# Optimization experiments

Measured on AMD Instinct MI355X. Metric: run time of the kernel, lower is better.

The kernel has to match this reference:

```python
import jax, jax.numpy as jnp
import numpy as np

EPS = 1e-12  # torch F.normalize eps

def _l2norm(x, axis):
    n = jnp.sqrt(jnp.sum(x * x, axis=axis, keepdims=True))
    return x / jnp.maximum(n, EPS)

def setup_inputs() -> dict:
    key = jax.random.key(0)
    k1, k2, k3, k4 = jax.random.split(key, 4)
    B, Lq, Ld, D, NWAY = 128, 32, 180, 128, 8
    query_reps = jax.random.normal(k1, (B, Lq, D), dtype=jnp.float32)
    doc_reps = jax.random.normal(k2, (B, NWAY, Ld, D), dtype=jnp.float32)
    doc_mask = jax.random.randint(k3, (B, NWAY, Ld), 0, 2, dtype=jnp.int32)
    # labels are teacher log-probabilities (KLDivLoss log_target=True)
    labels = jax.nn.log_softmax(jax.random.normal(k4, (B, NWAY), dtype=jnp.float32), axis=-1)
    return {"query_reps": query_reps, "doc_reps": doc_reps, "doc_mask": doc_mask, "labels": labels}

def reference(query_reps, doc_reps, doc_mask, labels):
    # query: L2-normalize over feature dim (dim=2 in torch call)
    q = _l2norm(query_reps, axis=-1)                      # [B, Lq, D]
    # docs: mask padding tokens, then F.normalize with DEFAULT dim=1,
    # i.e. L2-normalize along the token axis (faithful to source).
    d = doc_reps * doc_mask[..., None].astype(doc_reps.dtype)  # [B, W, Ld, D]
    d = _l2norm(d, axis=2)
    # MaxSim: sim[b,w,q,l] = <q_bq, d_bwl>; max over doc tokens, sum over query tokens
    sim = jnp.einsum('bqd,bwld->bwql', q, d)              # [B, W, Lq, Ld]
    scores = jnp.max(sim, axis=-1).sum(axis=-1)           # [B, W]
    log_p = jax.nn.log_softmax(scores, axis=-1)           # == log(softmax(scores))
    # KLDivLoss(log_target=True, reduction='batchmean'): sum(exp(t)*(t - x)) / B
    B = scores.shape[0]
    loss = jnp.sum(jnp.exp(labels) * (labels - log_p)) / B
    return loss  # torch.mean of a scalar is the scalar
```

## Files before the change

### kernel.cpp

```cpp
#include <hip/hip_runtime.h>
#include <math.h>

#define NB 128
#define LQ 32
#define LD 180
#define DD 128
#define NW 8
#define NBW (NB*NW)
#define TP 36

__global__ __launch_bounds__(256) void dnorm_kernel(
    const float* __restrict__ dreps, const int* __restrict__ dmask,
    float* __restrict__ dinv)
{
    __shared__ float s_ssq[8 * DD];
    const int t = threadIdx.x, bw = blockIdx.x;
    const float4* doc4 = (const float4*)(dreps + (size_t)bw * LD * DD);
    const int* mrow = dmask + bw * LD;
    const int d4 = t & 31, rg = t >> 5;
    float sx = 0.f, sy = 0.f, sz = 0.f, sw = 0.f;
    for (int l = rg; l < LD; l += 8) {
        float4 v = doc4[l * 32 + d4];
        float m = (float)mrow[l];
        sx += m * v.x * v.x; sy += m * v.y * v.y;
        sz += m * v.z * v.z; sw += m * v.w * v.w;
    }
    float4 ss; ss.x = sx; ss.y = sy; ss.z = sz; ss.w = sw;
    *(float4*)&s_ssq[rg * DD + 4 * d4] = ss;
    __syncthreads();
    if (t < DD) {
        float tot = 0.f;
        #pragma unroll
        for (int g = 0; g < 8; ++g) tot += s_ssq[g * DD + t];
        dinv[bw * DD + t] = 1.0f / fmaxf(sqrtf(tot), 1e-12f);
    }
}

__global__ __launch_bounds__(256) void qnorm_kernel(
    const float* __restrict__ qreps, float* __restrict__ qinv)
{
    const int t = threadIdx.x, b = blockIdx.x;
    const int r = t >> 3, sub = t & 7;
    const float4* qr = (const float4*)(qreps + (size_t)b * LQ * DD + r * DD + sub * 16);
    float ss = 0.f;
    #pragma unroll
    for (int k = 0; k < 4; ++k) {
        float4 v = qr[k];
        ss += v.x * v.x + v.y * v.y + v.z * v.z + v.w * v.w;
    }
    ss += __shfl_xor(ss, 4);
    ss += __shfl_xor(ss, 2);
    ss += __shfl_xor(ss, 1);
    if (sub == 0) qinv[b * LQ + r] = 1.0f / fmaxf(sqrtf(ss), 1e-12f);
}

__global__ __launch_bounds__(128, 2) void maxsim_kernel(
    const float* __restrict__ qreps, const float* __restrict__ dreps,
    const int* __restrict__ dmask, const float* __restrict__ dinv,
    const float* __restrict__ qinv, float* __restrict__ scores)
{
    __shared__ float s_tile[LD * TP];
    __shared__ float s_q[LQ * TP];
    __shared__ float s_pm[2][LQ];

    const int t = threadIdx.x, bw = blockIdx.x, b = bw >> 3;
    const int lane = t & 63, wave = t >> 6;
    const int rowg = lane >> 4;
    const int colg = lane & 15;
    const int colbase = wave * 84;

    const float4* doc4  = (const float4*)(dreps + (size_t)bw * LD * DD);
    const float4* q4g   = (const float4*)(qreps + (size_t)b * LQ * DD);
    const float4* dinv4 = (const float4*)(dinv + (size_t)bw * DD);
    const float*  qinvb = qinv + b * LQ;

    float acc[8][6];
    #pragma unroll
    for (int k = 0; k < 8; ++k)
        #pragma unroll
        for (int c = 0; c < 6; ++c) acc[k][c] = 0.f;

    for (int cc = 0; cc < 4; ++cc) {
        if (cc) __syncthreads();
        {
            int f = t;
            #pragma unroll
            for (int s = 0; s < 2; ++s, f += 128) {
                int r = f >> 3, d4 = f & 7;
                float4 v  = q4g[r * 32 + cc * 8 + d4];
                float4 di = dinv4[cc * 8 + d4];
                float  qi = qinvb[r];
                v.x *= qi * di.x; v.y *= qi * di.y;
                v.z *= qi * di.z; v.w *= qi * di.w;
                *(float4*)&s_q[r * TP + 4 * d4] = v;
            }
        }
        {
            int f = t;
            #pragma unroll
            for (int s = 0; s < 12; ++s, f += 128) {
                if (f < LD * 8) {
                    int l = f >> 3, d4 = f & 7;
                    *(float4*)&s_tile[l * TP + 4 * d4] = doc4[l * 32 + cc * 8 + d4];
                }
            }
        }
        __syncthreads();

        #pragma unroll
        for (int dq = 0; dq < 8; ++dq) {
            float4 qv[8], tv[6];
            #pragma unroll
            for (int k = 0; k < 8; ++k)
                qv[k] = *(const float4*)&s_q[(rowg + 4 * k) * TP + 4 * dq];
            #pragma unroll
            for (int c = 0; c < 6; ++c)
                tv[c] = *(const float4*)&s_tile[(colbase + colg + 16 * c) * TP + 4 * dq];
            #pragma unroll
            for (int k = 0; k < 8; ++k)
                #pragma unroll
                for (int c = 0; c < 6; ++c) {
                    acc[k][c] = fmaf(qv[k].x, tv[c].x, acc[k][c]);
                    acc[k][c] = fmaf(qv[k].y, tv[c].y, acc[k][c]);
                    acc[k][c] = fmaf(qv[k].z, tv[c].z, acc[k][c]);
                    acc[k][c] = fmaf(qv[k].w, tv[c].w, acc[k][c]);
                }
        }
    }

    int msk[6];
    #pragma unroll
    for (int c = 0; c < 6; ++c)
        msk[c] = dmask[bw * LD + colbase + colg + 16 * c];

    float pm[8];
    #pragma unroll
    for (int k = 0; k < 8; ++k) {
        float m = -INFINITY;
        #pragma unroll
        for (int c = 0; c < 6; ++c) {
            float cand = msk[c] ? acc[k][c] : 0.0f;
            m = fmaxf(m, cand);
        }
        pm[k] = m;
    }
    #pragma unroll
    for (int off = 8; off >= 1; off >>= 1)
        #pragma unroll
        for (int k = 0; k < 8; ++k)
            pm[k] = fmaxf(pm[k], __shfl_xor(pm[k], off));
    if (colg == 0) {
        #pragma unroll
        for (int k = 0; k < 8; ++k) s_pm[wave][rowg + 4 * k] = pm[k];
    }
    __syncthreads();
    if (t < LQ) {
        float v = fmaxf(s_pm[0][t], s_pm[1][t]);
        #pragma unroll
        for (int off = 16; off >= 1; off >>= 1) v += __shfl_xor(v, off);
        if (t == 0) scores[bw] = v;
    }
}

__global__ __launch_bounds__(NB) void finish_kernel(
    const float* __restrict__ scores, const float* __restrict__ labels,
    float* __restrict__ out)
{
    __shared__ float s_part[2];
    const int t = threadIdx.x;
    const float* sr = scores + t * NW;
    const float* lr = labels + t * NW;

    float s[NW];
    float m = -INFINITY;
    #pragma unroll
    for (int w = 0; w < NW; ++w) { s[w] = sr[w]; m = fmaxf(m, s[w]); }
    float se = 0.f;
    #pragma unroll
    for (int w = 0; w < NW; ++w) se += expf(s[w] - m);
    float lse = logf(se) + m;

    float term = 0.f;
    #pragma unroll
    for (int w = 0; w < NW; ++w) {
        float lw = lr[w];
        term += expf(lw) * (lw - (s[w] - lse));
    }
    #pragma unroll
    for (int off = 32; off > 0; off >>= 1) term += __shfl_xor(term, off);
    if ((t & 63) == 0) s_part[t >> 6] = term;
    __syncthreads();
    if (t == 0) out[0] = (s_part[0] + s_part[1]) / (float)NB;
}

extern "C" void kernel_launch(void* const* d_in, const int* in_sizes, int n_in,
                              void* d_out, int out_size, void* d_ws, size_t ws_size,
                              hipStream_t stream) {
    const float* qreps  = (const float*)d_in[0];
    const float* dreps  = (const float*)d_in[1];
    const int*   dmask  = (const int*)d_in[2];
    const float* labels = (const float*)d_in[3];
    float* out = (float*)d_out;

    float* scores = (float*)d_ws;
    float* dinv   = scores + NBW;
    float* qinv   = dinv + (size_t)NBW * DD;

    dnorm_kernel<<<NBW, 256, 0, stream>>>(dreps, dmask, dinv);
    qnorm_kernel<<<NB, 256, 0, stream>>>(qreps, qinv);
    maxsim_kernel<<<NBW, 128, 0, stream>>>(qreps, dreps, dmask, dinv, qinv, scores);
    finish_kernel<<<1, NB, 0, stream>>>(scores, labels, out);
}
```

Before: 188.4 us.

## Fuse doc token-axis normalization into maxsim kernel to avoid second doc read

Removes the separate dnorm kernel and computes the per-feature inverse norm inside maxsim. Each 32-feature chunk of the masked doc tile is already staged in shared memory, so the sum of squares is accumulated during the load. The resulting dinv is then applied to the query tile. Masking is applied to the doc values at load time, so the later mask check in the max reduction is dropped. This eliminates a full extra pass over the large doc tensor (about 94 MB) at the cost of two extra block barriers per chunk.

```diff
diff --git a/kernel.cpp b/kernel.cpp
--- a/kernel.cpp
+++ b/kernel.cpp
@@ -9,33 +9,6 @@
 #define NBW (NB*NW)
 #define TP 36
 
-__global__ __launch_bounds__(256) void dnorm_kernel(
-    const float* __restrict__ dreps, const int* __restrict__ dmask,
-    float* __restrict__ dinv)
-{
-    __shared__ float s_ssq[8 * DD];
-    const int t = threadIdx.x, bw = blockIdx.x;
-    const float4* doc4 = (const float4*)(dreps + (size_t)bw * LD * DD);
-    const int* mrow = dmask + bw * LD;
-    const int d4 = t & 31, rg = t >> 5;
-    float sx = 0.f, sy = 0.f, sz = 0.f, sw = 0.f;
-    for (int l = rg; l < LD; l += 8) {
-        float4 v = doc4[l * 32 + d4];
-        float m = (float)mrow[l];
-        sx += m * v.x * v.x; sy += m * v.y * v.y;
-        sz += m * v.z * v.z; sw += m * v.w * v.w;
-    }
-    float4 ss; ss.x = sx; ss.y = sy; ss.z = sz; ss.w = sw;
-    *(float4*)&s_ssq[rg * DD + 4 * d4] = ss;
-    __syncthreads();
-    if (t < DD) {
-        float tot = 0.f;
-        #pragma unroll
-        for (int g = 0; g < 8; ++g) tot += s_ssq[g * DD + t];
-        dinv[bw * DD + t] = 1.0f / fmaxf(sqrtf(tot), 1e-12f);
-    }
-}
-
 __global__ __launch_bounds__(256) void qnorm_kernel(
     const float* __restrict__ qreps, float* __restrict__ qinv)
 {
@@ -56,11 +29,13 @@
 
 __global__ __launch_bounds__(128, 2) void maxsim_kernel(
     const float* __restrict__ qreps, const float* __restrict__ dreps,
-    const int* __restrict__ dmask, const float* __restrict__ dinv,
-    const float* __restrict__ qinv, float* __restrict__ scores)
+    const int* __restrict__ dmask, const float* __restrict__ qinv,
+    float* __restrict__ scores)
 {
     __shared__ float s_tile[LD * TP];
     __shared__ float s_q[LQ * TP];
+    __shared__ float s_ssq[16 * 32];
+    __shared__ float s_dinv[32];
     __shared__ float s_pm[2][LQ];
 
     const int t = threadIdx.x, bw = blockIdx.x, b = bw >> 3;
@@ -71,8 +46,18 @@
 
     const float4* doc4  = (const float4*)(dreps + (size_t)bw * LD * DD);
     const float4* q4g   = (const float4*)(qreps + (size_t)b * LQ * DD);
-    const float4* dinv4 = (const float4*)(dinv + (size_t)bw * DD);
     const float*  qinvb = qinv + b * LQ;
+    const int*    mrow  = dmask + bw * LD;
+
+    const int d4 = t & 7;
+    const int rbase = t >> 3;
+
+    float mk[12];
+    #pragma unroll
+    for (int s = 0; s < 12; ++s) {
+        int l = rbase + 16 * s;
+        mk[s] = (l < LD) ? (float)mrow[l] : 0.0f;
+    }
 
     float acc[8][6];
     #pragma unroll
@@ -82,27 +67,49 @@
 
     for (int cc = 0; cc < 4; ++cc) {
         if (cc) __syncthreads();
+
         {
-            int f = t;
-            #pragma unroll
-            for (int s = 0; s < 2; ++s, f += 128) {
-                int r = f >> 3, d4 = f & 7;
-                float4 v  = q4g[r * 32 + cc * 8 + d4];
-                float4 di = dinv4[cc * 8 + d4];
-                float  qi = qinvb[r];
-                v.x *= qi * di.x; v.y *= qi * di.y;
-                v.z *= qi * di.z; v.w *= qi * di.w;
+            #pragma unroll
+            for (int s = 0; s < 2; ++s) {
+                int r = rbase + 16 * s;
+                float4 v = q4g[r * 32 + cc * 8 + d4];
+                float qi = qinvb[r];
+                v.x *= qi; v.y *= qi; v.z *= qi; v.w *= qi;
                 *(float4*)&s_q[r * TP + 4 * d4] = v;
             }
         }
+        float4 pssq = make_float4(0.f, 0.f, 0.f, 0.f);
+        #pragma unroll
+        for (int s = 0; s < 12; ++s) {
+            int l = rbase + 16 * s;
+            if (s < 11 || t < 32) {
+                float4 v = doc4[l * 32 + cc * 8 + d4];
+                float m = mk[s];
+                v.x *= m; v.y *= m; v.z *= m; v.w *= m;
+                pssq.x += v.x * v.x; pssq.y += v.y * v.y;
+                pssq.z += v.z * v.z; pssq.w += v.w * v.w;
+                *(float4*)&s_tile[l * TP + 4 * d4] = v;
+            }
+        }
+        *(float4*)&s_ssq[rbase * 32 + 4 * d4] = pssq;
+        __syncthreads();
+
+        if (t < 32) {
+            float tot = 0.f;
+            #pragma unroll
+            for (int g = 0; g < 16; ++g) tot += s_ssq[g * 32 + t];
+            s_dinv[t] = 1.0f / fmaxf(sqrtf(tot), 1e-12f);
+        }
+        __syncthreads();
+
         {
-            int f = t;
-            #pragma unroll
-            for (int s = 0; s < 12; ++s, f += 128) {
-                if (f < LD * 8) {
-                    int l = f >> 3, d4 = f & 7;
-                    *(float4*)&s_tile[l * TP + 4 * d4] = doc4[l * 32 + cc * 8 + d4];
-                }
+            float4 di = *(const float4*)&s_dinv[4 * d4];
+            #pragma unroll
+            for (int s = 0; s < 2; ++s) {
+                int r = rbase + 16 * s;
+                float4 v = *(float4*)&s_q[r * TP + 4 * d4];
+                v.x *= di.x; v.y *= di.y; v.z *= di.z; v.w *= di.w;
+                *(float4*)&s_q[r * TP + 4 * d4] = v;
             }
         }
         __syncthreads();
@@ -128,20 +135,12 @@
         }
     }
 
-    int msk[6];
-    #pragma unroll
-    for (int c = 0; c < 6; ++c)
-        msk[c] = dmask[bw * LD + colbase + colg + 16 * c];
-
     float pm[8];
     #pragma unroll
     for (int k = 0; k < 8; ++k) {
-        float m = -INFINITY;
-        #pragma unroll
-        for (int c = 0; c < 6; ++c) {
-            float cand = msk[c] ? acc[k][c] : 0.0f;
-            m = fmaxf(m, cand);
-        }
+        float m = acc[k][0];
+        #pragma unroll
+        for (int c = 1; c < 6; ++c) m = fmaxf(m, acc[k][c]);
         pm[k] = m;
     }
     #pragma unroll
@@ -203,11 +202,9 @@
     float* out = (float*)d_out;
 
     float* scores = (float*)d_ws;
-    float* dinv   = scores + NBW;
-    float* qinv   = dinv + (size_t)NBW * DD;
-
-    dnorm_kernel<<<NBW, 256, 0, stream>>>(dreps, dmask, dinv);
+    float* qinv   = scores + NBW;
+
     qnorm_kernel<<<NB, 256, 0, stream>>>(qreps, qinv);
-    maxsim_kernel<<<NBW, 128, 0, stream>>>(qreps, dreps, dmask, dinv, qinv, scores);
+    maxsim_kernel<<<NBW, 128, 0, stream>>>(qreps, dreps, dmask, qinv, scores);
     finish_kernel<<<1, NB, 0, stream>>>(scores, labels, out);
 }
```

New measurement: 180.9 us. -4.0%, faster.
